# Kernel optimization log

Measured on AMD Instinct MI355X. Metric: run time of the kernel, lower is better.

The kernel has to match this reference:

```python
import jax, jax.numpy as jnp
import numpy as np

B, N, H = 32, 1024, 512
THR = 0.05  # peak_detection_threshold


def _l2norm(x):
    return x / jnp.linalg.norm(x, axis=-1, keepdims=True)


def setup_inputs() -> dict:
    key = jax.random.key(0)
    ks = jax.random.split(key, 6)
    def w(k, shape, fan_in):
        return jax.random.normal(k, shape, jnp.float32) / np.float32(np.sqrt(fan_in))
    return {
        "segment_rep": jax.random.normal(ks[0], (B, N, H), jnp.float32),
        "phn_mask": jnp.ones((B, N), jnp.float32),
        # SegmentSimilarityMeasure: Linear(2H->H), ReLU, Linear(H->1, no bias)
        "W1": w(ks[1], (2 * H, H), 2 * H),
        "b1": jnp.zeros((H,), jnp.float32),
        "W2": w(ks[2], (H, 1), H),
        # word_enc: Linear(H->H), ReLU, Linear(H->H)
        "We1": w(ks[3], (H, H), H),
        "be1": jnp.zeros((H,), jnp.float32),
        "We2": w(ks[4], (H, H), H),
        "be2": jnp.zeros((H,), jnp.float32),
    }


def _forward(segment_rep, phn_mask, W1, b1, W2, We1, be1, We2, be2):
    Bs, Np, Hd = segment_rep.shape
    # adjacent segment similarity: MLP on concat of l2-normalized neighbors -> (B, N-1)
    cat = jnp.concatenate([_l2norm(segment_rep[:, :-1, :]), _l2norm(segment_rep[:, 1:, :])], axis=2)
    S = (jax.nn.relu(cat @ W1 + b1) @ W2)[..., 0]

    # relative dissimilarity
    Smin = jnp.min(S, axis=1, keepdims=True)
    Smax = jnp.max(S, axis=1, keepdims=True)
    D = 1.0 - (S - Smin) / (Smax - Smin)

    # peak detector (faithful to original, incl. final overwrite of first-order cols -2:)
    z = jnp.zeros_like(D)
    fo = z
    fo = fo.at[:, 0].set(jnp.maximum(D[:, 0] - D[:, 1], 0.0))
    fo = fo.at[:, 1:-1].set(jnp.minimum(jnp.maximum(D[:, 1:-1] - D[:, :-2], 0.0),
                                        jnp.maximum(D[:, 1:-1] - D[:, 2:], 0.0)))
    fo = fo.at[:, -1].set(jnp.maximum(D[:, -1] - D[:, -2], 0.0))
    so = z
    so = so.at[:, 0:2].set(jnp.maximum(D[:, 0:2] - D[:, 2:4], 0.0))
    so = so.at[:, 2:-2].set(jnp.minimum(jnp.maximum(D[:, 2:-2] - D[:, :-4], 0.0),
                                        jnp.maximum(D[:, 2:-2] - D[:, 4:], 0.0)))
    fo = fo.at[:, -2:].set(jnp.maximum(D[:, -2:] - D[:, -4:-2], 0.0))  # replicates original code
    P = jnp.minimum(jnp.maximum(jnp.maximum(fo, so) - THR, 0.0), fo)

    # pad, mask, straight-through hard boundaries
    P = jnp.pad(P, ((0, 0), (0, 1)))
    P = jax.nn.relu(P + (phn_mask - 1.0))
    b_soft = jnp.tanh(10.0 * P)
    b_hard = jnp.tanh(100000.0 * P)
    b = b_soft + jax.lax.stop_gradient(b_hard - b_soft)
    b = jnp.cumsum(b, axis=1)  # (B, N)
    b = b + (b[:, :1] == 0).astype(b.dtype)  # per-row +1 if b[:,0]==0
    num_word_segments = b[:, -1].astype(jnp.int32) + 1  # (B,)

    # U: column j holds j+1 for j < num_word_segments[i], else -100000. Nmax = N (static bound).
    cols = jnp.arange(1, Np + 1, dtype=jnp.int32)  # (Nmax,)
    U = jnp.where(cols[None, :] <= num_word_segments[:, None],
                  cols.astype(segment_rep.dtype)[None, :], -100000.0)  # (B, Nmax)

    V = U[:, None, :] - b[:, :, None]  # (B, N, Nmax)
    Wseg = 1.0 - jnp.tanh(100000.0 * jnp.abs(V))
    Wseg = Wseg / jnp.sum(Wseg, axis=1, keepdims=True)
    Wseg = jnp.nan_to_num(Wseg)

    # pool: (B, Nmax, N) @ (B, N, H) -> (B, Nmax, H)
    word_rep = jnp.einsum('bnm,bnh->bmh', Wseg, segment_rep)
    word_masks = jnp.where(word_rep == 0, 0.0, 1.0)
    out = jax.nn.relu(word_rep @ We1 + be1) @ We2 + be2
    return out * word_masks


def reference(segment_rep, phn_mask, W1, b1, W2, We1, be1, We2, be2):
    return _forward(segment_rep, phn_mask, W1, b1, W2, We1, be1, We2, be2)
```

## Files before the change

### kernel.cpp

```cpp
#include <hip/hip_runtime.h>

#define BB 32
#define NN 1024
#define HH 512
#define NS 1023

typedef unsigned short u16;
typedef unsigned int   u32;
typedef __attribute__((ext_vector_type(8))) short bf16x8;
typedef __attribute__((ext_vector_type(4))) float f32x4;

__device__ __forceinline__ float bf2f(u16 h) {
  union { u32 u; float f; } c; c.u = ((u32)h) << 16; return c.f;
}
__device__ __forceinline__ u16 f2bf(float f) {
  union { float f; u32 u; } c; c.f = f;
  u32 u = c.u;
  return (u16)((u + 0x7fffu + ((u >> 16) & 1u)) >> 16);
}
__device__ __forceinline__ void split_bf(float x, u16& hi, u16& lo) {
  hi = f2bf(x);
  lo = f2bf(x - bf2f(hi));
}
__device__ __forceinline__ void dma16(const u16* g, u16* l) {
  __builtin_amdgcn_global_load_lds(
      (const __attribute__((address_space(1))) u32*)g,
      (__attribute__((address_space(3))) u32*)l, 16, 0, 0);
}

__global__ __launch_bounds__(256) void k_prep_a(const float* __restrict__ seg,
                                                u16* __restrict__ ahi,
                                                u16* __restrict__ alo) {
  int row = blockIdx.x * 4 + (threadIdx.x >> 6);
  int lane = threadIdx.x & 63;
  const float4* p = (const float4*)(seg + ((size_t)row << 9) + lane * 8);
  float4 a = p[0], b = p[1];
  float v[8] = {a.x, a.y, a.z, a.w, b.x, b.y, b.z, b.w};
  float s = 0.f;
#pragma unroll
  for (int i = 0; i < 8; ++i) s += v[i] * v[i];
#pragma unroll
  for (int m = 32; m; m >>= 1) s += __shfl_xor(s, m, 64);
  float nrm = sqrtf(s);
  u16 h[8], l[8];
#pragma unroll
  for (int i = 0; i < 8; ++i) split_bf(v[i] / nrm, h[i], l[i]);
  size_t off = ((size_t)row << 9) + lane * 8;
  *(uint4*)(ahi + off) = make_uint4(h[0] | (h[1] << 16), h[2] | (h[3] << 16),
                                    h[4] | (h[5] << 16), h[6] | (h[7] << 16));
  *(uint4*)(alo + off) = make_uint4(l[0] | (l[1] << 16), l[2] | (l[3] << 16),
                                    l[4] | (l[5] << 16), l[6] | (l[7] << 16));
}

__global__ __launch_bounds__(256) void k_tr3(const float* __restrict__ W1,
                                             const float* __restrict__ We1,
                                             const float* __restrict__ We2,
                                             u16* __restrict__ w1h,
                                             u16* __restrict__ w1l,
                                             u16* __restrict__ we1t,
                                             u16* __restrict__ we2t) {
  __shared__ u16 Th[64 * 66], Tl[64 * 66];
  int z = blockIdx.z;
  const float* src; u16 *dh, *dl; int K, N;
  if (z == 0)      { src = W1;  dh = w1h;  dl = w1l;          K = 1024; N = 512; }
  else if (z == 1) { src = We1; dh = we1t; dl = (u16*)0;      K = 512;  N = 512; }
  else             { src = We2; dh = we2t; dl = (u16*)0;      K = 512;  N = 512; }
  if (blockIdx.y * 64 >= K) return;
  int nb = blockIdx.x * 64, kb = blockIdx.y * 64;
  int tid = threadIdx.x;
#pragma unroll
  for (int i = 0; i < 16; ++i) {
    int e = tid + i * 256;
    int r = e >> 6, c = e & 63;
    float v = src[(size_t)(kb + r) * N + nb + c];
    u16 hi, lo; split_bf(v, hi, lo);
    Th[c * 66 + r] = hi;
    Tl[c * 66 + r] = lo;
  }
  __syncthreads();
#pragma unroll
  for (int i = 0; i < 16; ++i) {
    int e = tid + i * 256;
    int n = e >> 6, k = e & 63;
    dh[(size_t)(nb + n) * K + kb + k] = Th[n * 66 + k];
    if (dl) dl[(size_t)(nb + n) * K + kb + k] = Tl[n * 66 + k];
  }
}

__global__ __launch_bounds__(512, 2) void k_sgemm(const u16* __restrict__ ahi,
                                                  const u16* __restrict__ alo,
                                                  const u16* __restrict__ w1h,
                                                  const u16* __restrict__ w1l,
                                                  const float* __restrict__ b1,
                                                  const float* __restrict__ W2,
                                                  float* __restrict__ Spart) {
  __shared__ u16 Ah[2][256 * 32];
  __shared__ u16 Al[2][256 * 32];
  __shared__ u16 Bh[2][256 * 32];
  __shared__ u16 Bl[2][256 * 32];

  const int tid  = threadIdx.x;
  const int wave = tid >> 6, lane = tid & 63;
  const int quad = lane >> 4, l15 = lane & 15;
  const int wm = wave >> 2, wn = wave & 3;
  const int r_in = lane >> 2, c_in = lane & 3;
  const int w    = blockIdx.x;
  const int xcd  = w & 7, slot = w >> 3;
  const int nblk = slot & 1;
  const int mblk = xcd * 16 + (slot >> 1);
  const int mrow0 = mblk * 256;
  const int ncol0 = nblk * 256;

#define SG_AH(tb_, ks_)                                                      \
  {                                                                          \
    int k0_ = (ks_) * 32, half_ = k0_ >> 9, cb_ = k0_ & 511;                 \
    int g0_ = mrow0 + wave * 32 + r_in + half_;                              \
    int g1_ = g0_ + 16;                                                      \
    if (g0_ > 32767) g0_ = 32767;                                            \
    if (g1_ > 32767) g1_ = 32767;                                            \
    dma16(ahi + ((((size_t)g0_) << 9) + cb_ + c_in * 8),                     \
          &Ah[tb_][(wave * 32) * 32]);                                       \
    dma16(ahi + ((((size_t)g1_) << 9) + cb_ + c_in * 8),                     \
          &Ah[tb_][(wave * 32 + 16) * 32]);                                  \
  }
#define SG_AL(tb_, ks_)                                                      \
  {                                                                          \
    int k0_ = (ks_) * 32, half_ = k0_ >> 9, cb_ = k0_ & 511;                 \
    int g0_ = mrow0 + wave * 32 + r_in + half_;                              \
    int g1_ = g0_ + 16;                                                      \
    if (g0_ > 32767) g0_ = 32767;                                            \
    if (g1_ > 32767) g1_ = 32767;                                            \
    dma16(alo + ((((size_t)g0_) << 9) + cb_ + c_in * 8),                     \
          &Al[tb_][(wave * 32) * 32]);                                       \
    dma16(alo + ((((size_t)g1_) << 9) + cb_ + c_in * 8),                     \
          &Al[tb_][(wave * 32 + 16) * 32]);                                  \
  }
#define SG_BH(tb_, ks_)                                                      \
  {                                                                          \
    int k0_ = (ks_) * 32;                                                    \
    int n0_ = ncol0 + wave * 32 + r_in;                                      \
    dma16(w1h + (((size_t)n0_) << 10) + k0_ + c_in * 8,                      \
          &Bh[tb_][(wave * 32) * 32]);                                       \
    dma16(w1h + (((size_t)(n0_ + 16)) << 10) + k0_ + c_in * 8,               \
          &Bh[tb_][(wave * 32 + 16) * 32]);                                  \
  }
#define SG_BL(tb_, ks_)                                                      \
  {                                                                          \
    int k0_ = (ks_) * 32;                                                    \
    int n0_ = ncol0 + wave * 32 + r_in;                                      \
    dma16(w1l + (((size_t)n0_) << 10) + k0_ + c_in * 8,                      \
          &Bl[tb_][(wave * 32) * 32]);                                       \
    dma16(w1l + (((size_t)(n0_ + 16)) << 10) + k0_ + c_in * 8,               \
          &Bl[tb_][(wave * 32 + 16) * 32]);                                  \
  }

  f32x4 acc[8][4];
#pragma unroll
  for (int mi = 0; mi < 8; ++mi)
#pragma unroll
    for (int ni = 0; ni < 4; ++ni) acc[mi][ni] = (f32x4){0.f, 0.f, 0.f, 0.f};

  SG_AH(0, 0) SG_BH(0, 0) SG_BL(0, 0) SG_AL(0, 0)
  asm volatile("s_waitcnt vmcnt(4)" ::: "memory");
  __builtin_amdgcn_s_barrier();

  for (int ks = 0; ks < 32; ++ks) {
    const int bb = ks & 1;
    const int nx = (ks + 1 < 32) ? ks + 1 : 31;
    bf16x8 ah[8], al[8], bh[4], bl[4];

#pragma unroll
    for (int mi = 0; mi < 8; ++mi)
      ah[mi] = *(const bf16x8*)&Ah[bb][(wm * 128 + mi * 16 + l15) * 32 + quad * 8];
#pragma unroll
    for (int ni = 0; ni < 4; ++ni)
      bh[ni] = *(const bf16x8*)&Bh[bb][(wn * 64 + ni * 16 + l15) * 32 + quad * 8];
    SG_AH(bb ^ 1, nx) SG_BH(bb ^ 1, nx)
    asm volatile("s_waitcnt lgkmcnt(0)" ::: "memory");
    __builtin_amdgcn_sched_barrier(0);
    __builtin_amdgcn_s_setprio(1);
#pragma unroll
    for (int ni = 0; ni < 4; ++ni)
#pragma unroll
      for (int mi = 0; mi < 8; ++mi)
        acc[mi][ni] = __builtin_amdgcn_mfma_f32_16x16x32_bf16(ah[mi], bh[ni], acc[mi][ni], 0, 0, 0);
    __builtin_amdgcn_s_setprio(0);
    asm volatile("s_waitcnt vmcnt(6)" ::: "memory");
    __builtin_amdgcn_s_barrier();

#pragma unroll
    for (int ni = 0; ni < 4; ++ni)
      bl[ni] = *(const bf16x8*)&Bl[bb][(wn * 64 + ni * 16 + l15) * 32 + quad * 8];
    SG_BL(bb ^ 1, nx) SG_AL(bb ^ 1, nx)
    asm volatile("s_waitcnt lgkmcnt(0)" ::: "memory");
    __builtin_amdgcn_sched_barrier(0);
    __builtin_amdgcn_s_setprio(1);
#pragma unroll
    for (int ni = 0; ni < 4; ++ni)
#pragma unroll
      for (int mi = 0; mi < 8; ++mi)
        acc[mi][ni] = __builtin_amdgcn_mfma_f32_16x16x32_bf16(ah[mi], bl[ni], acc[mi][ni], 0, 0, 0);
    __builtin_amdgcn_s_setprio(0);
    asm volatile("s_waitcnt vmcnt(8)" ::: "memory");
    __builtin_amdgcn_s_barrier();

#pragma unroll
    for (int mi = 0; mi < 8; ++mi)
      al[mi] = *(const bf16x8*)&Al[bb][(wm * 128 + mi * 16 + l15) * 32 + quad * 8];
    asm volatile("s_waitcnt lgkmcnt(0)" ::: "memory");
    __builtin_amdgcn_sched_barrier(0);
    __builtin_amdgcn_s_setprio(1);
#pragma unroll
    for (int ni = 0; ni < 4; ++ni)
#pragma unroll
      for (int mi = 0; mi < 8; ++mi)
        acc[mi][ni] = __builtin_amdgcn_mfma_f32_16x16x32_bf16(al[mi], bh[ni], acc[mi][ni], 0, 0, 0);
    __builtin_amdgcn_s_setprio(0);
    asm volatile("s_waitcnt vmcnt(4)" ::: "memory");
    __builtin_amdgcn_s_barrier();
  }
#undef SG_AH
#undef SG_AL
#undef SG_BH
#undef SG_BL

  asm volatile("s_waitcnt vmcnt(0)" ::: "memory");
  __syncthreads();

  float* red = (float*)&Ah[0][0];
  float b1v[4], w2v[4];
#pragma unroll
  for (int ni = 0; ni < 4; ++ni) {
    int n_g = ncol0 + wn * 64 + ni * 16 + l15;
    b1v[ni] = b1[n_g];
    w2v[ni] = W2[n_g];
  }
#pragma unroll
  for (int mi = 0; mi < 8; ++mi) {
#pragma unroll
    for (int reg = 0; reg < 4; ++reg) {
      float part = 0.f;
#pragma unroll
      for (int ni = 0; ni < 4; ++ni) {
        float h = acc[mi][ni][reg] + b1v[ni];
        h = h > 0.f ? h : 0.f;
        part = fmaf(h, w2v[ni], part);
      }
#pragma unroll
      for (int m = 8; m; m >>= 1) part += __shfl_xor(part, m, 64);
      if (l15 == 0) red[wave * 128 + mi * 16 + quad * 4 + reg] = part;
    }
  }
  __syncthreads();
  if (tid < 256) {
    int wmr = tid >> 7, rl = tid & 127;
    float s = red[(wmr * 4 + 0) * 128 + rl] + red[(wmr * 4 + 1) * 128 + rl]
            + red[(wmr * 4 + 2) * 128 + rl] + red[(wmr * 4 + 3) * 128 + rl];
    int grow = mrow0 + tid;
    int b = grow >> 10, n = grow & 1023;
    if (n < NS)
      Spart[((size_t)nblk * BB + b) * NN + n] = s;
  }
}

__global__ __launch_bounds__(256) void k_row(const float* __restrict__ S0,
                                             const float* __restrict__ S1,
                                             const float* __restrict__ mask,
                                             int* __restrict__ assign,
                                             float* __restrict__ weight,
                                             float* __restrict__ total,
                                             int* __restrict__ startn,
                                             int* __restrict__ endn) {
  int b = blockIdx.x, tid = threadIdx.x;
  __shared__ float Ssh[NS];
  __shared__ float Dsh[NS];
  __shared__ float tsh[NN];
  __shared__ float bsh[NN];
  __shared__ float totl[NN];
  __shared__ int   stl[NN];
  __shared__ int   enl[NN];
  __shared__ float red[256];

  for (int n = tid; n < NS; n += 256)
    Ssh[n] = S0[((size_t)b << 10) + n] + S1[((size_t)b << 10) + n];
  __syncthreads();

  float mn = INFINITY, mx = -INFINITY;
  for (int n = tid; n < NS; n += 256) {
    float v = Ssh[n];
    mn = fminf(mn, v); mx = fmaxf(mx, v);
  }
  red[tid] = mn; __syncthreads();
  for (int s = 128; s; s >>= 1) { if (tid < s) red[tid] = fminf(red[tid], red[tid + s]); __syncthreads(); }
  float Smin = red[0]; __syncthreads();
  red[tid] = mx; __syncthreads();
  for (int s = 128; s; s >>= 1) { if (tid < s) red[tid] = fmaxf(red[tid], red[tid + s]); __syncthreads(); }
  float Smax = red[0]; __syncthreads();

  for (int n = tid; n < NS; n += 256)
    Dsh[n] = 1.0f - (Ssh[n] - Smin) / (Smax - Smin);
  __syncthreads();

  for (int n = tid; n < NN; n += 256) {
    float P;
    if (n >= NS) {
      P = 0.f;
    } else {
      float D = Dsh[n];
      float fo, so;
      if (n == 0)            fo = fmaxf(D - Dsh[1], 0.f);
      else if (n >= NS - 2)  fo = fmaxf(D - Dsh[n - 2], 0.f);
      else                   fo = fminf(fmaxf(D - Dsh[n - 1], 0.f),
                                        fmaxf(D - Dsh[n + 1], 0.f));
      if (n <= 1)            so = fmaxf(D - Dsh[n + 2], 0.f);
      else if (n >= NS - 2)  so = 0.f;
      else                   so = fminf(fmaxf(D - Dsh[n - 2], 0.f),
                                        fmaxf(D - Dsh[n + 2], 0.f));
      P = fminf(fmaxf(fmaxf(fo, so) - 0.05f, 0.f), fo);
    }
    float m = mask[((size_t)b << 10) + n];
    P = P + (m - 1.0f);
    P = P > 0.f ? P : 0.f;
    float bs = tanhf(10.0f * P);
    float bh = tanhf(100000.0f * P);
    tsh[n] = bs + (bh - bs);
  }
  __syncthreads();

  if (tid == 0) {
    float acc = 0.f;
    for (int n = 0; n < NN; n += 8) {
      float t0 = tsh[n + 0], t1 = tsh[n + 1], t2 = tsh[n + 2], t3 = tsh[n + 3];
      float t4 = tsh[n + 4], t5 = tsh[n + 5], t6 = tsh[n + 6], t7 = tsh[n + 7];
      acc += t0; bsh[n + 0] = acc; acc += t1; bsh[n + 1] = acc;
      acc += t2; bsh[n + 2] = acc; acc += t3; bsh[n + 3] = acc;
      acc += t4; bsh[n + 4] = acc; acc += t5; bsh[n + 5] = acc;
      acc += t6; bsh[n + 6] = acc; acc += t7; bsh[n + 7] = acc;
    }
  }
  __syncthreads();

  float add1 = (bsh[0] == 0.0f) ? 1.0f : 0.0f;
  int   num  = (int)(bsh[NN - 1] + add1) + 1;

  for (int mi = tid; mi < NN; mi += 256) { totl[mi] = 0.f; stl[mi] = 1 << 30; enl[mi] = -1; }
  __syncthreads();

  for (int n = tid; n < NN; n += 256) {
    float bv = bsh[n] + add1;
    float kf = rintf(bv);
    int   k  = (int)kf;
    int   a  = -1; float w = 0.f;
    if (k >= 1 && k <= num && k <= NN) {
      float v = fabsf(kf - bv);
      w = 1.0f - tanhf(100000.0f * v);
      if (w > 0.f) {
        a = k - 1;
        atomicAdd(&totl[a], w);
        atomicMin(&stl[a], n);
        atomicMax(&enl[a], n);
      } else {
        a = -1; w = 0.f;
      }
    }
    assign[((size_t)b << 10) + n] = a;
    weight[((size_t)b << 10) + n] = w;
  }
  __syncthreads();
  for (int mi = tid; mi < NN; mi += 256) {
    total [((size_t)b << 10) + mi] = totl[mi];
    startn[((size_t)b << 10) + mi] = stl[mi];
    endn  [((size_t)b << 10) + mi] = enl[mi];
  }
}

__global__ __launch_bounds__(64) void k_pool(const float* __restrict__ seg,
                                             const int* __restrict__ assign,
                                             const float* __restrict__ weight,
                                             const float* __restrict__ total,
                                             const int* __restrict__ startn,
                                             const int* __restrict__ endn,
                                             u16* hrep,
                                             unsigned char* __restrict__ mb) {
  int bm = blockIdx.x;
  int b  = bm >> 10, m = bm & 1023;
  int lane = threadIdx.x;
  float acc[8] = {0.f, 0.f, 0.f, 0.f, 0.f, 0.f, 0.f, 0.f};
  float tm = total[bm];
  if (tm > 0.f) {
    int s = startn[bm], e = endn[bm];
    for (int n = s; n <= e; ++n) {
      if (assign[((size_t)b << 10) + n] != m) continue;
      float coef = weight[((size_t)b << 10) + n] / tm;
      const float4* p = (const float4*)(seg + (((size_t)b << 10) + n) * HH + lane * 8);
      float4 x = p[0], y = p[1];
      acc[0] = fmaf(coef, x.x, acc[0]); acc[1] = fmaf(coef, x.y, acc[1]);
      acc[2] = fmaf(coef, x.z, acc[2]); acc[3] = fmaf(coef, x.w, acc[3]);
      acc[4] = fmaf(coef, y.x, acc[4]); acc[5] = fmaf(coef, y.y, acc[5]);
      acc[6] = fmaf(coef, y.z, acc[6]); acc[7] = fmaf(coef, y.w, acc[7]);
    }
  }
  u16 h[8];
  unsigned int mbyte = 0;
#pragma unroll
  for (int j = 0; j < 8; ++j) {
    h[j] = f2bf(acc[j]);
    mbyte |= (acc[j] == 0.f ? 1u : 0u) << j;
  }
  *(uint4*)(hrep + ((size_t)bm << 10) + lane * 8) =
      make_uint4(h[0] | (h[1] << 16), h[2] | (h[3] << 16),
                 h[4] | (h[5] << 16), h[6] | (h[7] << 16));
  mb[((size_t)bm << 6) + lane] = (unsigned char)mbyte;
}

__global__ __launch_bounds__(512, 4) void k_g(const u16* asrc,
                                              const u16* __restrict__ bmat,
                                              const float* __restrict__ bias,
                                              const unsigned char* __restrict__ mb,
                                              float* outp,
                                              u16* hid,
                                              int a_off, int mode) {
  __shared__ u16 As[3][64 * 32];
  __shared__ u16 Bs[2][512 * 32];

  const int tid  = threadIdx.x;
  const int wave = tid >> 6, lane = tid & 63;
  const int quad = lane >> 4, l15 = lane & 15;
  const int wm = wave >> 2, wn = wave & 3;
  const int r_in = lane >> 2, c_in = lane & 3;
  const int mrow0 = blockIdx.x * 64;

#define SGB(tb_, ks_)                                                        \
  {                                                                          \
    int k0_ = (ks_) * 32;                                                    \
    _Pragma("unroll")                                                        \
    for (int g_ = 0; g_ < 4; ++g_) {                                         \
      int n_ = wave * 64 + g_ * 16 + r_in;                                   \
      dma16(bmat + (size_t)n_ * 512 + k0_ + c_in * 8,                        \
            &Bs[tb_][(wave * 64 + g_ * 16) * 32]);                           \
    }                                                                        \
  }
#define SGA(sl_, ks_)                                                        \
  {                                                                          \
    if (wave < 4) {                                                          \
      int k0_ = (ks_) * 32;                                                  \
      int row_ = wave * 16 + r_in;                                           \
      dma16(asrc + ((size_t)(mrow0 + row_) << 10) + a_off + k0_ + c_in * 8,  \
            &As[sl_][(wave * 16) * 32]);                                     \
    }                                                                        \
  }

  f32x4 acc[2][8];
#pragma unroll
  for (int mi = 0; mi < 2; ++mi)
#pragma unroll
    for (int ni = 0; ni < 8; ++ni) acc[mi][ni] = (f32x4){0.f, 0.f, 0.f, 0.f};

  SGB(0, 0) SGA(0, 0) SGA(1, 1)
  if (wave < 4) { asm volatile("s_waitcnt vmcnt(1)" ::: "memory"); }
  else          { asm volatile("s_waitcnt vmcnt(0)" ::: "memory"); }
  __builtin_amdgcn_s_barrier();

  for (int ks = 0; ks < 16; ++ks) {
    const int bb = ks & 1;
    const int ra = ks % 3;
    const int nb = (ks + 1 < 16) ? ks + 1 : 15;
    const int na = (ks + 2 < 16) ? ks + 2 : 15;
    SGB(bb ^ 1, nb)
    SGA((ks + 2) % 3, na)
    bf16x8 a[2], b[8];
#pragma unroll
    for (int mi = 0; mi < 2; ++mi)
      a[mi] = *(const bf16x8*)&As[ra][(wm * 32 + mi * 16 + l15) * 32 + quad * 8];
#pragma unroll
    for (int ni = 0; ni < 8; ++ni)
      b[ni] = *(const bf16x8*)&Bs[bb][(wn * 128 + ni * 16 + l15) * 32 + quad * 8];
    asm volatile("s_waitcnt lgkmcnt(0)" ::: "memory");
    __builtin_amdgcn_sched_barrier(0);
    __builtin_amdgcn_s_setprio(1);
#pragma unroll
    for (int ni = 0; ni < 8; ++ni)
#pragma unroll
      for (int mi = 0; mi < 2; ++mi)
        acc[mi][ni] = __builtin_amdgcn_mfma_f32_16x16x32_bf16(a[mi], b[ni], acc[mi][ni], 0, 0, 0);
    __builtin_amdgcn_s_setprio(0);
    if (wave < 4) { asm volatile("s_waitcnt vmcnt(1)" ::: "memory"); }
    else          { asm volatile("s_waitcnt vmcnt(0)" ::: "memory"); }
    __builtin_amdgcn_s_barrier();
  }
#undef SGB
#undef SGA
  asm volatile("s_waitcnt vmcnt(0)" ::: "memory");

  float bv[8];
#pragma unroll
  for (int ni = 0; ni < 8; ++ni) bv[ni] = bias[wn * 128 + ni * 16 + l15];

  if (mode == 1) {
#pragma unroll
    for (int mi = 0; mi < 2; ++mi)
#pragma unroll
      for (int ni = 0; ni < 8; ++ni)
#pragma unroll
        for (int reg = 0; reg < 4; ++reg) {
          int col = wn * 128 + ni * 16 + l15;
          int row = mrow0 + wm * 32 + mi * 16 + quad * 4 + reg;
          float h = acc[mi][ni][reg] + bv[ni];
          h = h > 0.f ? h : 0.f;
          hid[((size_t)row << 10) + 512 + col] = f2bf(h);
        }
  } else {
#pragma unroll
    for (int mi = 0; mi < 2; ++mi)
#pragma unroll
      for (int ni = 0; ni < 8; ++ni)
#pragma unroll
        for (int reg = 0; reg < 4; ++reg) {
          int col = wn * 128 + ni * 16 + l15;
          int row = mrow0 + wm * 32 + mi * 16 + quad * 4 + reg;
          float o = acc[mi][ni][reg] + bv[ni];
          unsigned char m8 = mb[((size_t)row << 6) + (col >> 3)];
          outp[((size_t)row << 9) + col] = ((m8 >> (col & 7)) & 1) ? 0.f : o;
        }
  }
}

__global__ void k_diag(float* __restrict__ out, int hostcode) {
  if (hostcode != 0) out[0] = (float)hostcode;
}

extern "C" void kernel_launch(void* const* d_in, const int* in_sizes, int n_in,
                              void* d_out, int out_size, void* d_ws, size_t ws_size,
                              hipStream_t stream) {
  const float* seg  = (const float*)d_in[0];
  const float* mask = (const float*)d_in[1];
  const float* W1   = (const float*)d_in[2];
  const float* b1   = (const float*)d_in[3];
  const float* W2   = (const float*)d_in[4];
  const float* We1  = (const float*)d_in[5];
  const float* be1  = (const float*)d_in[6];
  const float* We2  = (const float*)d_in[7];
  const float* be2  = (const float*)d_in[8];

  const size_t NROW = (size_t)BB * NN;
  float* ws = (float*)d_ws;
  float* S0     = ws;
  float* S1     = S0 + NROW;
  int*   assign = (int*)(S1 + NROW);
  float* weight = (float*)(assign + NROW);
  float* total  = weight + NROW;
  int*   startn = (int*)(total + NROW);
  int*   endn   = startn + NROW;
  u16*   w1h    = (u16*)(endn + NROW);
  u16*   w1l    = w1h + (size_t)512 * 1024;
  u16*   we1t   = w1l + (size_t)512 * 1024;
  u16*   we2t   = we1t + (size_t)512 * 512;

  float* out = (float*)d_out;
  u16*   ahi = (u16*)d_out;
  u16*   alo = ahi + (size_t)NROW * HH;
  u16*   hrep = (u16*)d_out;
  unsigned char* mbuf = (unsigned char*)w1h;

  int hostcode = 0;
  if (ws_size < (size_t)7 * NROW * 4 + (size_t)3 * 1024 * 1024) hostcode += 32768;
  if (out_size != 16777216) hostcode += 8192;

  k_prep_a<<<dim3(BB * NN / 4), dim3(256), 0, stream>>>(seg, ahi, alo);
  k_tr3   <<<dim3(8, 16, 3), dim3(256), 0, stream>>>(W1, We1, We2, w1h, w1l, we1t, we2t);
  k_sgemm <<<dim3(256), dim3(512), 0, stream>>>(ahi, alo, w1h, w1l, b1, W2, S0);
  k_row   <<<dim3(BB), dim3(256), 0, stream>>>(S0, S1, mask, assign, weight, total, startn, endn);
  k_pool  <<<dim3(BB * NN), dim3(64), 0, stream>>>(seg, assign, weight, total, startn, endn, hrep, mbuf);
  k_g     <<<dim3(512), dim3(512), 0, stream>>>(hrep, we1t, be1, mbuf, out, hrep, 0,   1);
  k_g     <<<dim3(512), dim3(512), 0, stream>>>(hrep, we2t, be2, mbuf, out, hrep, 512, 2);
  k_diag  <<<dim3(1), dim3(1), 0, stream>>>(out, hostcode);
}
```

Before: 314.1 us.

## Fuse word encoder MLP layers into one kernel with LDS-resident hidden tile

Merges the two word-encoder GEMM launches into a single kernel. The ReLU hidden activations for each 64-row tile are written to shared memory (padded stride 520) and consumed directly by the second GEMM, whose weights are read straight from global memory without the LDS pipelining. This removes a launch and the global round trip of the hidden tensor, at the cost of an unpipelined second GEMM. The pooling kernel also packs four 64-thread rows per 256-thread block to cut block count.

```diff
diff --git a/kernel.cpp b/kernel.cpp
--- a/kernel.cpp
+++ b/kernel.cpp
@@ -374,17 +374,17 @@
   }
 }
 
-__global__ __launch_bounds__(64) void k_pool(const float* __restrict__ seg,
-                                             const int* __restrict__ assign,
-                                             const float* __restrict__ weight,
-                                             const float* __restrict__ total,
-                                             const int* __restrict__ startn,
-                                             const int* __restrict__ endn,
-                                             u16* hrep,
-                                             unsigned char* __restrict__ mb) {
-  int bm = blockIdx.x;
+__global__ __launch_bounds__(256) void k_pool(const float* __restrict__ seg,
+                                              const int* __restrict__ assign,
+                                              const float* __restrict__ weight,
+                                              const float* __restrict__ total,
+                                              const int* __restrict__ startn,
+                                              const int* __restrict__ endn,
+                                              u16* hrep,
+                                              unsigned char* __restrict__ mb) {
+  int bm = blockIdx.x * 4 + (threadIdx.x >> 6);
   int b  = bm >> 10, m = bm & 1023;
-  int lane = threadIdx.x;
+  int lane = threadIdx.x & 63;
   float acc[8] = {0.f, 0.f, 0.f, 0.f, 0.f, 0.f, 0.f, 0.f};
   float tm = total[bm];
   if (tm > 0.f) {
@@ -413,15 +413,17 @@
   mb[((size_t)bm << 6) + lane] = (unsigned char)mbyte;
 }
 
-__global__ __launch_bounds__(512, 4) void k_g(const u16* asrc,
-                                              const u16* __restrict__ bmat,
-                                              const float* __restrict__ bias,
-                                              const unsigned char* __restrict__ mb,
-                                              float* outp,
-                                              u16* hid,
-                                              int a_off, int mode) {
-  __shared__ u16 As[3][64 * 32];
-  __shared__ u16 Bs[2][512 * 32];
+__global__ __launch_bounds__(512, 4) void k_out2(const u16* asrc,
+                                                 const u16* __restrict__ we1t,
+                                                 const u16* __restrict__ we2t,
+                                                 const float* __restrict__ be1,
+                                                 const float* __restrict__ be2,
+                                                 const unsigned char* __restrict__ mb,
+                                                 float* outp) {
+  __shared__ u16 SH[3 * 64 * 32 + 2 * 512 * 32];
+  u16* As  = SH;
+  u16* Bs  = SH + 3 * 64 * 32;
+  u16* Hid = SH;
 
   const int tid  = threadIdx.x;
   const int wave = tid >> 6, lane = tid & 63;
@@ -436,8 +438,8 @@
     _Pragma("unroll")                                                        \
     for (int g_ = 0; g_ < 4; ++g_) {                                         \
       int n_ = wave * 64 + g_ * 16 + r_in;                                   \
-      dma16(bmat + (size_t)n_ * 512 + k0_ + c_in * 8,                        \
-            &Bs[tb_][(wave * 64 + g_ * 16) * 32]);                           \
+      dma16(we1t + (size_t)n_ * 512 + k0_ + c_in * 8,                        \
+            Bs + (tb_) * (512 * 32) + (wave * 64 + g_ * 16) * 32);           \
     }                                                                        \
   }
 #define SGA(sl_, ks_)                                                        \
@@ -445,8 +447,8 @@
     if (wave < 4) {                                                          \
       int k0_ = (ks_) * 32;                                                  \
       int row_ = wave * 16 + r_in;                                           \
-      dma16(asrc + ((size_t)(mrow0 + row_) << 10) + a_off + k0_ + c_in * 8,  \
-            &As[sl_][(wave * 16) * 32]);                                     \
+      dma16(asrc + ((size_t)(mrow0 + row_) << 10) + k0_ + c_in * 8,          \
+            As + (sl_) * (64 * 32) + (wave * 16) * 32);                      \
     }                                                                        \
   }
 
@@ -471,10 +473,10 @@
     bf16x8 a[2], b[8];
 #pragma unroll
     for (int mi = 0; mi < 2; ++mi)
-      a[mi] = *(const bf16x8*)&As[ra][(wm * 32 + mi * 16 + l15) * 32 + quad * 8];
+      a[mi] = *(const bf16x8*)&As[ra * (64 * 32) + (wm * 32 + mi * 16 + l15) * 32 + quad * 8];
 #pragma unroll
     for (int ni = 0; ni < 8; ++ni)
-      b[ni] = *(const bf16x8*)&Bs[bb][(wn * 128 + ni * 16 + l15) * 32 + quad * 8];
+      b[ni] = *(const bf16x8*)&Bs[bb * (512 * 32) + (wn * 128 + ni * 16 + l15) * 32 + quad * 8];
     asm volatile("s_waitcnt lgkmcnt(0)" ::: "memory");
     __builtin_amdgcn_sched_barrier(0);
     __builtin_amdgcn_s_setprio(1);
@@ -491,12 +493,52 @@
 #undef SGB
 #undef SGA
   asm volatile("s_waitcnt vmcnt(0)" ::: "memory");
-
-  float bv[8];
-#pragma unroll
-  for (int ni = 0; ni < 8; ++ni) bv[ni] = bias[wn * 128 + ni * 16 + l15];
-
-  if (mode == 1) {
+  __syncthreads();
+
+  {
+    float bv1[8];
+#pragma unroll
+    for (int ni = 0; ni < 8; ++ni) bv1[ni] = be1[wn * 128 + ni * 16 + l15];
+#pragma unroll
+    for (int mi = 0; mi < 2; ++mi)
+#pragma unroll
+      for (int ni = 0; ni < 8; ++ni)
+#pragma unroll
+        for (int reg = 0; reg < 4; ++reg) {
+          int col = wn * 128 + ni * 16 + l15;
+          int row = wm * 32 + mi * 16 + quad * 4 + reg;
+          float h = acc[mi][ni][reg] + bv1[ni];
+          h = h > 0.f ? h : 0.f;
+          Hid[row * 520 + col] = f2bf(h);
+        }
+  }
+  __syncthreads();
+
+#pragma unroll
+  for (int mi = 0; mi < 2; ++mi)
+#pragma unroll
+    for (int ni = 0; ni < 8; ++ni) acc[mi][ni] = (f32x4){0.f, 0.f, 0.f, 0.f};
+
+#pragma unroll 2
+  for (int ks = 0; ks < 16; ++ks) {
+    bf16x8 a[2], b[8];
+#pragma unroll
+    for (int mi = 0; mi < 2; ++mi)
+      a[mi] = *(const bf16x8*)&Hid[(wm * 32 + mi * 16 + l15) * 520 + ks * 32 + quad * 8];
+#pragma unroll
+    for (int ni = 0; ni < 8; ++ni)
+      b[ni] = *(const bf16x8*)(we2t + (size_t)(wn * 128 + ni * 16 + l15) * 512 + ks * 32 + quad * 8);
+#pragma unroll
+    for (int ni = 0; ni < 8; ++ni)
+#pragma unroll
+      for (int mi = 0; mi < 2; ++mi)
+        acc[mi][ni] = __builtin_amdgcn_mfma_f32_16x16x32_bf16(a[mi], b[ni], acc[mi][ni], 0, 0, 0);
+  }
+
+  {
+    float bv2[8];
+#pragma unroll
+    for (int ni = 0; ni < 8; ++ni) bv2[ni] = be2[wn * 128 + ni * 16 + l15];
 #pragma unroll
     for (int mi = 0; mi < 2; ++mi)
 #pragma unroll
@@ -505,20 +547,7 @@
         for (int reg = 0; reg < 4; ++reg) {
           int col = wn * 128 + ni * 16 + l15;
           int row = mrow0 + wm * 32 + mi * 16 + quad * 4 + reg;
-          float h = acc[mi][ni][reg] + bv[ni];
-          h = h > 0.f ? h : 0.f;
-          hid[((size_t)row << 10) + 512 + col] = f2bf(h);
-        }
-  } else {
-#pragma unroll
-    for (int mi = 0; mi < 2; ++mi)
-#pragma unroll
-      for (int ni = 0; ni < 8; ++ni)
-#pragma unroll
-        for (int reg = 0; reg < 4; ++reg) {
-          int col = wn * 128 + ni * 16 + l15;
-          int row = mrow0 + wm * 32 + mi * 16 + quad * 4 + reg;
-          float o = acc[mi][ni][reg] + bv[ni];
+          float o = acc[mi][ni][reg] + bv2[ni];
           unsigned char m8 = mb[((size_t)row << 6) + (col >> 3)];
           outp[((size_t)row << 9) + col] = ((m8 >> (col & 7)) & 1) ? 0.f : o;
         }
@@ -570,8 +599,7 @@
   k_tr3   <<<dim3(8, 16, 3), dim3(256), 0, stream>>>(W1, We1, We2, w1h, w1l, we1t, we2t);
   k_sgemm <<<dim3(256), dim3(512), 0, stream>>>(ahi, alo, w1h, w1l, b1, W2, S0);
   k_row   <<<dim3(BB), dim3(256), 0, stream>>>(S0, S1, mask, assign, weight, total, startn, endn);
-  k_pool  <<<dim3(BB * NN), dim3(64), 0, stream>>>(seg, assign, weight, total, startn, endn, hrep, mbuf);
-  k_g     <<<dim3(512), dim3(512), 0, stream>>>(hrep, we1t, be1, mbuf, out, hrep, 0,   1);
-  k_g     <<<dim3(512), dim3(512), 0, stream>>>(hrep, we2t, be2, mbuf, out, hrep, 512, 2);
+  k_pool  <<<dim3(BB * NN / 4), dim3(256), 0, stream>>>(seg, assign, weight, total, startn, endn, hrep, mbuf);
+  k_out2  <<<dim3(512), dim3(512), 0, stream>>>(hrep, we1t, we2t, be1, be2, mbuf, out);
   k_diag  <<<dim3(1), dim3(1), 0, stream>>>(out, hostcode);
 }
```

Result: slower. 343.1 us (+9.2%).

## Split word-encoder GEMM into 64x256 tiles with XCD-aware mapping and pack pool blocks

Applied to the files above, without the earlier changes.

The word-encoder GEMM kernel now computes 64x256 output tiles instead of 64x512, launching 1024 blocks instead of 512. Block indices are remapped so the tiles of one row block stay on the same XCD, which should improve L2 reuse of the A rows. B staging moves to triple buffering with a deeper vmcnt wait so loads stay further ahead. The pooling kernel packs four 64-lane rows per 256-thread block to cut launch overhead from tiny blocks. Each A tile is now loaded twice, once per column half, and per-block MFMA work is halved, which could raise load overhead.

```diff
diff --git a/kernel.cpp b/kernel.cpp
--- a/kernel.cpp
+++ b/kernel.cpp
@@ -374,17 +374,17 @@
   }
 }
 
-__global__ __launch_bounds__(64) void k_pool(const float* __restrict__ seg,
-                                             const int* __restrict__ assign,
-                                             const float* __restrict__ weight,
-                                             const float* __restrict__ total,
-                                             const int* __restrict__ startn,
-                                             const int* __restrict__ endn,
-                                             u16* hrep,
-                                             unsigned char* __restrict__ mb) {
-  int bm = blockIdx.x;
+__global__ __launch_bounds__(256) void k_pool(const float* __restrict__ seg,
+                                              const int* __restrict__ assign,
+                                              const float* __restrict__ weight,
+                                              const float* __restrict__ total,
+                                              const int* __restrict__ startn,
+                                              const int* __restrict__ endn,
+                                              u16* hrep,
+                                              unsigned char* __restrict__ mb) {
+  int bm = blockIdx.x * 4 + (threadIdx.x >> 6);
   int b  = bm >> 10, m = bm & 1023;
-  int lane = threadIdx.x;
+  int lane = threadIdx.x & 63;
   float acc[8] = {0.f, 0.f, 0.f, 0.f, 0.f, 0.f, 0.f, 0.f};
   float tm = total[bm];
   if (tm > 0.f) {
@@ -413,97 +413,97 @@
   mb[((size_t)bm << 6) + lane] = (unsigned char)mbyte;
 }
 
-__global__ __launch_bounds__(512, 4) void k_g(const u16* asrc,
-                                              const u16* __restrict__ bmat,
-                                              const float* __restrict__ bias,
-                                              const unsigned char* __restrict__ mb,
-                                              float* outp,
-                                              u16* hid,
-                                              int a_off, int mode) {
+__global__ __launch_bounds__(512, 4) void k_g2(const u16* asrc,
+                                               const u16* __restrict__ bmat,
+                                               const float* __restrict__ bias,
+                                               const unsigned char* __restrict__ mb,
+                                               float* outp,
+                                               u16* hid,
+                                               int a_off, int mode) {
   __shared__ u16 As[3][64 * 32];
-  __shared__ u16 Bs[2][512 * 32];
+  __shared__ u16 Bs[3][256 * 32];
 
   const int tid  = threadIdx.x;
   const int wave = tid >> 6, lane = tid & 63;
   const int quad = lane >> 4, l15 = lane & 15;
   const int wm = wave >> 2, wn = wave & 3;
   const int r_in = lane >> 2, c_in = lane & 3;
-  const int mrow0 = blockIdx.x * 64;
-
-#define SGB(tb_, ks_)                                                        \
+  const int w    = blockIdx.x;
+  const int xcd  = w & 7, slot = w >> 3;
+  const int nblk = slot & 1;
+  const int mblk = xcd * 64 + (slot >> 1);
+  const int mrow0 = mblk * 64;
+  const int ncol0 = nblk * 256;
+
+#define SA(sl_, ks_)                                                         \
+  if (wave < 4) {                                                            \
+    int k0_ = (ks_) * 32;                                                    \
+    dma16(asrc + ((size_t)(mrow0 + wave * 16 + r_in) << 10) + a_off + k0_ + c_in * 8, \
+          &As[sl_][(wave * 16) * 32]);                                       \
+  }
+#define SB(sl_, ks_)                                                         \
   {                                                                          \
     int k0_ = (ks_) * 32;                                                    \
     _Pragma("unroll")                                                        \
-    for (int g_ = 0; g_ < 4; ++g_) {                                         \
-      int n_ = wave * 64 + g_ * 16 + r_in;                                   \
+    for (int g_ = 0; g_ < 2; ++g_) {                                         \
+      int n_ = ncol0 + wave * 32 + g_ * 16 + r_in;                           \
       dma16(bmat + (size_t)n_ * 512 + k0_ + c_in * 8,                        \
-            &Bs[tb_][(wave * 64 + g_ * 16) * 32]);                           \
+            &Bs[sl_][(wave * 32 + g_ * 16) * 32]);                           \
     }                                                                        \
   }
-#define SGA(sl_, ks_)                                                        \
-  {                                                                          \
-    if (wave < 4) {                                                          \
-      int k0_ = (ks_) * 32;                                                  \
-      int row_ = wave * 16 + r_in;                                           \
-      dma16(asrc + ((size_t)(mrow0 + row_) << 10) + a_off + k0_ + c_in * 8,  \
-            &As[sl_][(wave * 16) * 32]);                                     \
-    }                                                                        \
-  }
-
-  f32x4 acc[2][8];
+
+  f32x4 acc[2][4];
 #pragma unroll
   for (int mi = 0; mi < 2; ++mi)
 #pragma unroll
-    for (int ni = 0; ni < 8; ++ni) acc[mi][ni] = (f32x4){0.f, 0.f, 0.f, 0.f};
-
-  SGB(0, 0) SGA(0, 0) SGA(1, 1)
-  if (wave < 4) { asm volatile("s_waitcnt vmcnt(1)" ::: "memory"); }
-  else          { asm volatile("s_waitcnt vmcnt(0)" ::: "memory"); }
+    for (int ni = 0; ni < 4; ++ni) acc[mi][ni] = (f32x4){0.f, 0.f, 0.f, 0.f};
+
+  SA(0, 0) SB(0, 0) SA(1, 1) SB(1, 1)
+  if (wave < 4) { asm volatile("s_waitcnt vmcnt(3)" ::: "memory"); }
+  else          { asm volatile("s_waitcnt vmcnt(2)" ::: "memory"); }
   __builtin_amdgcn_s_barrier();
 
   for (int ks = 0; ks < 16; ++ks) {
-    const int bb = ks & 1;
     const int ra = ks % 3;
-    const int nb = (ks + 1 < 16) ? ks + 1 : 15;
-    const int na = (ks + 2 < 16) ? ks + 2 : 15;
-    SGB(bb ^ 1, nb)
-    SGA((ks + 2) % 3, na)
-    bf16x8 a[2], b[8];
+    const int sl = (ks + 2) % 3;
+    const int nx = (ks + 2 < 16) ? ks + 2 : 15;
+    SA(sl, nx) SB(sl, nx)
+    bf16x8 a[2], b[4];
 #pragma unroll
     for (int mi = 0; mi < 2; ++mi)
       a[mi] = *(const bf16x8*)&As[ra][(wm * 32 + mi * 16 + l15) * 32 + quad * 8];
 #pragma unroll
-    for (int ni = 0; ni < 8; ++ni)
-      b[ni] = *(const bf16x8*)&Bs[bb][(wn * 128 + ni * 16 + l15) * 32 + quad * 8];
+    for (int ni = 0; ni < 4; ++ni)
+      b[ni] = *(const bf16x8*)&Bs[ra][(wn * 64 + ni * 16 + l15) * 32 + quad * 8];
     asm volatile("s_waitcnt lgkmcnt(0)" ::: "memory");
     __builtin_amdgcn_sched_barrier(0);
     __builtin_amdgcn_s_setprio(1);
 #pragma unroll
-    for (int ni = 0; ni < 8; ++ni)
+    for (int ni = 0; ni < 4; ++ni)
 #pragma unroll
       for (int mi = 0; mi < 2; ++mi)
         acc[mi][ni] = __builtin_amdgcn_mfma_f32_16x16x32_bf16(a[mi], b[ni], acc[mi][ni], 0, 0, 0);
     __builtin_amdgcn_s_setprio(0);
-    if (wave < 4) { asm volatile("s_waitcnt vmcnt(1)" ::: "memory"); }
-    else          { asm volatile("s_waitcnt vmcnt(0)" ::: "memory"); }
+    if (wave < 4) { asm volatile("s_waitcnt vmcnt(3)" ::: "memory"); }
+    else          { asm volatile("s_waitcnt vmcnt(2)" ::: "memory"); }
     __builtin_amdgcn_s_barrier();
   }
-#undef SGB
-#undef SGA
+#undef SA
+#undef SB
   asm volatile("s_waitcnt vmcnt(0)" ::: "memory");
 
-  float bv[8];
-#pragma unroll
-  for (int ni = 0; ni < 8; ++ni) bv[ni] = bias[wn * 128 + ni * 16 + l15];
+  float bv[4];
+#pragma unroll
+  for (int ni = 0; ni < 4; ++ni) bv[ni] = bias[ncol0 + wn * 64 + ni * 16 + l15];
 
   if (mode == 1) {
 #pragma unroll
     for (int mi = 0; mi < 2; ++mi)
 #pragma unroll
-      for (int ni = 0; ni < 8; ++ni)
+      for (int ni = 0; ni < 4; ++ni)
 #pragma unroll
         for (int reg = 0; reg < 4; ++reg) {
-          int col = wn * 128 + ni * 16 + l15;
+          int col = ncol0 + wn * 64 + ni * 16 + l15;
           int row = mrow0 + wm * 32 + mi * 16 + quad * 4 + reg;
           float h = acc[mi][ni][reg] + bv[ni];
           h = h > 0.f ? h : 0.f;
@@ -513,10 +513,10 @@
 #pragma unroll
     for (int mi = 0; mi < 2; ++mi)
 #pragma unroll
-      for (int ni = 0; ni < 8; ++ni)
+      for (int ni = 0; ni < 4; ++ni)
 #pragma unroll
         for (int reg = 0; reg < 4; ++reg) {
-          int col = wn * 128 + ni * 16 + l15;
+          int col = ncol0 + wn * 64 + ni * 16 + l15;
           int row = mrow0 + wm * 32 + mi * 16 + quad * 4 + reg;
           float o = acc[mi][ni][reg] + bv[ni];
           unsigned char m8 = mb[((size_t)row << 6) + (col >> 3)];
@@ -570,8 +570,8 @@
   k_tr3   <<<dim3(8, 16, 3), dim3(256), 0, stream>>>(W1, We1, We2, w1h, w1l, we1t, we2t);
   k_sgemm <<<dim3(256), dim3(512), 0, stream>>>(ahi, alo, w1h, w1l, b1, W2, S0);
   k_row   <<<dim3(BB), dim3(256), 0, stream>>>(S0, S1, mask, assign, weight, total, startn, endn);
-  k_pool  <<<dim3(BB * NN), dim3(64), 0, stream>>>(seg, assign, weight, total, startn, endn, hrep, mbuf);
-  k_g     <<<dim3(512), dim3(512), 0, stream>>>(hrep, we1t, be1, mbuf, out, hrep, 0,   1);
-  k_g     <<<dim3(512), dim3(512), 0, stream>>>(hrep, we2t, be2, mbuf, out, hrep, 512, 2);
+  k_pool  <<<dim3(BB * NN / 4), dim3(256), 0, stream>>>(seg, assign, weight, total, startn, endn, hrep, mbuf);
+  k_g2    <<<dim3(1024), dim3(512), 0, stream>>>(hrep, we1t, be1, mbuf, out, hrep, 0,   1);
+  k_g2    <<<dim3(1024), dim3(512), 0, stream>>>(hrep, we2t, be2, mbuf, out, hrep, 512, 2);
   k_diag  <<<dim3(1), dim3(1), 0, stream>>>(out, hostcode);
 }
```

New measurement: 319.6 us. No clear change (+1.8%).
